# Kernel optimization log

Hardware: AMD Instinct MI355X
Metric: run time of the kernel (lower is better)

## Reference

```python
import jax, jax.numpy as jnp
import numpy as np

B, DIM, K, NH = 65536, 8, 64, 100
TOTAL = DIM * K


def setup_inputs() -> dict:
    key = jax.random.key(0)
    ks = jax.random.split(key, 14)
    e = jax.random.normal(ks[0], (B, DIM, K), dtype=jnp.float32)
    # strictly upper-triangular DAG adjacency: C[j, i] = 1 iff j < i (j is a parent of i)
    C = jnp.triu(jnp.ones((DIM, DIM), dtype=jnp.int32), k=1)
    sc = 0.05
    inp = {"e": e, "C": C}
    inp["sW1"] = jax.random.normal(ks[1], (TOTAL, NH), dtype=jnp.float32) * sc
    inp["sb1"] = jnp.zeros((NH,), dtype=jnp.float32)
    inp["sW2"] = jax.random.normal(ks[2], (NH, NH), dtype=jnp.float32) * sc
    inp["sb2"] = jnp.zeros((NH,), dtype=jnp.float32)
    inp["sW3"] = jax.random.normal(ks[3], (NH, K), dtype=jnp.float32) * sc
    inp["sb3"] = jnp.zeros((K,), dtype=jnp.float32)
    inp["tW1"] = jax.random.normal(ks[4], (TOTAL, NH), dtype=jnp.float32) * sc
    inp["tb1"] = jnp.zeros((NH,), dtype=jnp.float32)
    inp["tW2"] = jax.random.normal(ks[5], (NH, NH), dtype=jnp.float32) * sc
    inp["tb2"] = jnp.zeros((NH,), dtype=jnp.float32)
    inp["tW3"] = jax.random.normal(ks[6], (NH, K), dtype=jnp.float32) * sc
    inp["tb3"] = jnp.zeros((K,), dtype=jnp.float32)
    return inp


def _mlp(x, mask, W1, b1, W2, b2, W3, b3):
    # MLP.forward: net(x * mask); Linear->ReLU->Linear->ReLU->Linear->Sigmoid
    h = jax.nn.relu((x * mask) @ W1 + b1)
    h = jax.nn.relu(h @ W2 + b2)
    return jax.nn.sigmoid(h @ W3 + b3)


def reference(e, C, sW1, sb1, sW2, sb2, sW3, sb3, tW1, tb1, tW2, tb2, tW3, tb3):
    b, dim, k = e.shape
    total = dim * k
    # mask for step i: column C[:, i] with each entry repeated k times -> [total]
    # (if column i is all zeros, mask is zeros, matching the elif branch)
    masks = jnp.repeat(C.astype(e.dtype), k, axis=0).T  # [dim, total]
    e_steps = jnp.swapaxes(e, 0, 1)  # [dim, B, k]

    def step(z, xs):
        i, mask, e_i = xs
        zf = z.reshape(b, total)
        s = _mlp(zf, mask, sW1, sb1, sW2, sb2, sW3, sb3)  # [B, k]
        t = _mlp(zf, mask, tW1, tb1, tW2, tb2, tW3, tb3)  # [B, k]
        z = z.at[:, i, :].set(jnp.exp(s) * e_i + t)
        return z, jnp.sum(s, axis=1)

    z0 = jnp.zeros_like(e)
    z, ld_steps = jax.lax.scan(step, z0, (jnp.arange(dim), masks, e_steps))
    log_det = jnp.sum(ld_steps, axis=0)  # [B]
    return z, log_det
```

## Files before the change

### kernel.cpp

```cpp
#include <hip/hip_runtime.h>

#define B_SZ 65536
#define NH   100

typedef __bf16 bf16_t;
typedef __bf16 bf16x2 __attribute__((ext_vector_type(2)));
typedef __bf16 bf16x8 __attribute__((ext_vector_type(8)));
typedef float  f32x4  __attribute__((ext_vector_type(4)));

#define SZ_W2 14336
#define SZ_W3 8192
#define SZ_W1 7168
#define OFF_W3   28672
#define OFF_W1   45056
#define WS_TOTAL 145408

__global__ void prep_weights(const float* __restrict__ sW1, const float* __restrict__ sW2,
                             const float* __restrict__ sW3, const float* __restrict__ tW1,
                             const float* __restrict__ tW2, const float* __restrict__ tW3,
                             bf16_t* __restrict__ ws) {
  int idx = blockIdx.x * 256 + threadIdx.x;
  if (idx >= WS_TOTAL) return;
  float v = 0.f;
  if (idx < 2 * SZ_W2) {
    const float* W = (idx < SZ_W2) ? sW2 : tW2;
    int l = (idx < SZ_W2) ? idx : idx - SZ_W2;
    int j = l & 7, ln = (l >> 3) & 63, kc = (l >> 9) & 3, mt = l >> 11;
    int k = kc * 32 + (ln >> 4) * 8 + j;
    int m = mt * 16 + (ln & 15);
    v = (k < NH && m < NH) ? W[k * NH + m] : 0.f;
  } else if (idx < OFF_W1) {
    int l = idx - OFF_W3;
    const float* W = (l < SZ_W3) ? sW3 : tW3;
    l &= (SZ_W3 - 1);
    int j = l & 7, ln = (l >> 3) & 63, kc = (l >> 9) & 3, mt = l >> 11;
    int k = kc * 32 + (ln >> 4) * 8 + j;
    int m = mt * 16 + (ln & 15);
    v = (k < NH) ? W[k * 64 + m] : 0.f;
  } else {
    int l = idx - OFF_W1;
    int b = l / (2 * SZ_W1);
    int r2 = l - b * 2 * SZ_W1;
    const float* W = (r2 < SZ_W1) ? sW1 : tW1;
    int w = (r2 < SZ_W1) ? r2 : r2 - SZ_W1;
    int j = w & 7, ln = (w >> 3) & 63, kc = (w >> 9) & 1, mt = w >> 10;
    int k = kc * 32 + (ln >> 4) * 8 + j;
    int m = mt * 16 + (ln & 15);
    v = (m < NH) ? W[(b * 64 + k) * NH + m] : 0.f;
  }
  ws[idx] = (bf16_t)v;
}

__global__ void prep_bias(const float* __restrict__ sb1, const float* __restrict__ sb2,
                          const float* __restrict__ sb3, const float* __restrict__ tb1,
                          const float* __restrict__ tb2, const float* __restrict__ tb3,
                          float* __restrict__ fb) {
  int t = threadIdx.x;
  if (t < 112)       fb[t] = (t < NH) ? sb2[t] : 0.f;
  else if (t < 224)  fb[t] = (t - 112 < NH) ? tb2[t - 112] : 0.f;
  else if (t < 288)  fb[t] = sb3[t - 224];
  else if (t < 352)  fb[t] = tb3[t - 288];
  else if (t < 464)  fb[t] = (t - 352 < NH) ? sb1[t - 352] : 0.f;
  else if (t < 576)  fb[t] = (t - 464 < NH) ? tb1[t - 464] : 0.f;
}

__device__ __forceinline__ void gload_lds16(const void* gptr, void* lptr) {
  __builtin_amdgcn_global_load_lds(
      (const __attribute__((address_space(1))) unsigned int*)gptr,
      (__attribute__((address_space(3))) unsigned int*)lptr, 16, 0, 0);
}

__device__ __forceinline__ unsigned pk2(float a, float b) {
  bf16x2 t = {(bf16_t)a, (bf16_t)b};
  return __builtin_bit_cast(unsigned, t);
}

__device__ __forceinline__ void plswap(unsigned &x, unsigned &y) {
  asm("v_permlane32_swap_b32 %0, %1" : "+v"(x), "+v"(y));
  asm("v_permlane16_swap_b32 %0, %1" : "+v"(x), "+v"(y));
}

__device__ __forceinline__ bf16x8 build_bfrag(unsigned lo0, unsigned lo1,
                                              unsigned hi0, unsigned hi1) {
  plswap(lo0, hi0);
  plswap(lo1, hi1);
  union { unsigned u[4]; bf16x8 v; } r;
  r.u[0] = lo0; r.u[1] = lo1; r.u[2] = hi0; r.u[3] = hi1;
  return r.v;
}

struct __align__(16) SMem {
  bf16_t w2[2 * SZ_W2];
  bf16_t w3[2 * SZ_W3];
  float  bias[512];
};

__global__ __launch_bounds__(512, 2) void flow_kernel(
    const float* __restrict__ e,
    const bf16_t* __restrict__ wf,
    const float* __restrict__ fb,
    float* __restrict__ out) {
  __shared__ SMem sm;

  const int tid  = threadIdx.x;
  const int wave = tid >> 6;
  const int lane = tid & 63;
  const int c    = lane & 15;
  const int Q    = lane >> 4;
  const int rowBase = blockIdx.x * 256 + wave * 32;

  {
    const char* g = (const char*)wf;
    char* l = (char*)&sm;
    const char* gb = (const char*)fb;
    #pragma unroll
    for (int t = 0; t < 12; ++t) {
      const int ch = t * 8 + wave;
      if (ch < 88)      gload_lds16(g + ch * 1024 + lane * 16, l + ch * 1024);
      else if (ch < 90) gload_lds16(gb + (ch - 88) * 1024 + lane * 16,
                                    (char*)sm.bias + (ch - 88) * 1024);
    }
  }

  f32x4 acc1S[2][7], acc1T[2][7];
  #pragma unroll
  for (int th = 0; th < 7; ++th) {
    const f32x4 vs = *(const f32x4*)(fb + 352 + th * 16 + Q * 4);
    const f32x4 vt = *(const f32x4*)(fb + 464 + th * 16 + Q * 4);
    acc1S[0][th] = vs; acc1S[1][th] = vs;
    acc1T[0][th] = vt; acc1T[1][th] = vt;
  }
  float ldacc[2] = {0.f, 0.f};

  __syncthreads();

  const float* lb2S = sm.bias;
  const float* lb2T = sm.bias + 112;
  const float* lb3S = sm.bias + 224;
  const float* lb3T = sm.bias + 288;

  auto run_net = [&](const f32x4 (&acc1)[2][7], const bf16_t* __restrict__ w2f,
                     const bf16_t* __restrict__ w3f, const float* __restrict__ lb2,
                     const float* __restrict__ lb3, f32x4 (&acc3)[2][4]) {
    unsigned pk[2][7][2];
    #pragma unroll
    for (int mt = 0; mt < 2; ++mt)
      #pragma unroll
      for (int th = 0; th < 7; ++th) {
        pk[mt][th][0] = pk2(fmaxf(acc1[mt][th][0], 0.f), fmaxf(acc1[mt][th][1], 0.f));
        pk[mt][th][1] = pk2(fmaxf(acc1[mt][th][2], 0.f), fmaxf(acc1[mt][th][3], 0.f));
      }
    f32x4 acc2[2][7];
    #pragma unroll
    for (int th = 0; th < 7; ++th) {
      const f32x4 bv = *(const f32x4*)(lb2 + th * 16 + Q * 4);
      acc2[0][th] = bv; acc2[1][th] = bv;
    }
    #pragma unroll
    for (int kc = 0; kc < 4; ++kc) {
      const int tlo = kc * 2, thi = (kc * 2 + 1 > 6) ? 6 : kc * 2 + 1;
      const bf16x8 b0 = build_bfrag(pk[0][tlo][0], pk[0][tlo][1], pk[0][thi][0], pk[0][thi][1]);
      const bf16x8 b1 = build_bfrag(pk[1][tlo][0], pk[1][tlo][1], pk[1][thi][0], pk[1][thi][1]);
      #pragma unroll
      for (int th = 0; th < 7; ++th) {
        const bf16x8 A = *(const bf16x8*)(w2f + ((th * 4 + kc) * 64 + lane) * 8);
        acc2[0][th] = __builtin_amdgcn_mfma_f32_16x16x32_bf16(A, b0, acc2[0][th], 0, 0, 0);
        acc2[1][th] = __builtin_amdgcn_mfma_f32_16x16x32_bf16(A, b1, acc2[1][th], 0, 0, 0);
      }
    }
    #pragma unroll
    for (int mt = 0; mt < 2; ++mt)
      #pragma unroll
      for (int th = 0; th < 7; ++th) {
        pk[mt][th][0] = pk2(fmaxf(acc2[mt][th][0], 0.f), fmaxf(acc2[mt][th][1], 0.f));
        pk[mt][th][1] = pk2(fmaxf(acc2[mt][th][2], 0.f), fmaxf(acc2[mt][th][3], 0.f));
      }
    #pragma unroll
    for (int ot = 0; ot < 4; ++ot) {
      const f32x4 bv = *(const f32x4*)(lb3 + ot * 16 + Q * 4);
      acc3[0][ot] = bv; acc3[1][ot] = bv;
    }
    #pragma unroll
    for (int kc = 0; kc < 4; ++kc) {
      const int tlo = kc * 2, thi = (kc * 2 + 1 > 6) ? 6 : kc * 2 + 1;
      const bf16x8 b0 = build_bfrag(pk[0][tlo][0], pk[0][tlo][1], pk[0][thi][0], pk[0][thi][1]);
      const bf16x8 b1 = build_bfrag(pk[1][tlo][0], pk[1][tlo][1], pk[1][thi][0], pk[1][thi][1]);
      #pragma unroll
      for (int ot = 0; ot < 4; ++ot) {
        const bf16x8 A = *(const bf16x8*)(w3f + ((ot * 4 + kc) * 64 + lane) * 8);
        acc3[0][ot] = __builtin_amdgcn_mfma_f32_16x16x32_bf16(A, b0, acc3[0][ot], 0, 0, 0);
        acc3[1][ot] = __builtin_amdgcn_mfma_f32_16x16x32_bf16(A, b1, acc3[1][ot], 0, 0, 0);
      }
    }
  };

  for (int i = 0; i < 8; ++i) {
    f32x4 acc3S[2][4], acc3T[2][4];
    run_net(acc1S, sm.w2,         sm.w3,         lb2S, lb3S, acc3S);
    run_net(acc1T, sm.w2 + SZ_W2, sm.w3 + SZ_W3, lb2T, lb3T, acc3T);

    unsigned zpk[2][4][2];
    #pragma unroll
    for (int mt = 0; mt < 2; ++mt) {
      #pragma unroll
      for (int ot = 0; ot < 4; ++ot) {
        const int off = (rowBase + mt * 16 + c) * 512 + i * 64 + ot * 16 + Q * 4;
        const f32x4 ev = *(const f32x4*)(e + off);
        f32x4 zv;
        float ss = 0.f;
        #pragma unroll
        for (int r = 0; r < 4; ++r) {
          const float sv = __builtin_amdgcn_rcpf(1.f + __expf(-acc3S[mt][ot][r]));
          const float tv = __builtin_amdgcn_rcpf(1.f + __expf(-acc3T[mt][ot][r]));
          zv[r] = __expf(sv) * ev[r] + tv;
          ss += sv;
        }
        __builtin_nontemporal_store(zv, (f32x4*)(out + off));
        zpk[mt][ot][0] = pk2(zv[0], zv[1]);
        zpk[mt][ot][1] = pk2(zv[2], zv[3]);
        ldacc[mt] += ss;
      }
    }

    if (i < 7) {
      const bf16_t* __restrict__ w1g = wf + OFF_W1 + i * 2 * SZ_W1;
      #pragma unroll
      for (int kc = 0; kc < 2; ++kc) {
        const bf16x8 b0 = build_bfrag(zpk[0][kc * 2][0], zpk[0][kc * 2][1],
                                      zpk[0][kc * 2 + 1][0], zpk[0][kc * 2 + 1][1]);
        const bf16x8 b1 = build_bfrag(zpk[1][kc * 2][0], zpk[1][kc * 2][1],
                                      zpk[1][kc * 2 + 1][0], zpk[1][kc * 2 + 1][1]);
        #pragma unroll
        for (int th = 0; th < 7; ++th) {
          const bf16x8 AS = *(const bf16x8*)(w1g + ((th * 2 + kc) * 64 + lane) * 8);
          const bf16x8 AT = *(const bf16x8*)(w1g + SZ_W1 + ((th * 2 + kc) * 64 + lane) * 8);
          acc1S[0][th] = __builtin_amdgcn_mfma_f32_16x16x32_bf16(AS, b0, acc1S[0][th], 0, 0, 0);
          acc1S[1][th] = __builtin_amdgcn_mfma_f32_16x16x32_bf16(AS, b1, acc1S[1][th], 0, 0, 0);
          acc1T[0][th] = __builtin_amdgcn_mfma_f32_16x16x32_bf16(AT, b0, acc1T[0][th], 0, 0, 0);
          acc1T[1][th] = __builtin_amdgcn_mfma_f32_16x16x32_bf16(AT, b1, acc1T[1][th], 0, 0, 0);
        }
      }
    }
  }

  #pragma unroll
  for (int mt = 0; mt < 2; ++mt) {
    float v = ldacc[mt];
    v += __shfl_xor(v, 16);
    v += __shfl_xor(v, 32);
    if (Q == 0) out[B_SZ * 512 + rowBase + mt * 16 + c] = v;
  }
}

extern "C" void kernel_launch(void* const* d_in, const int* in_sizes, int n_in,
                              void* d_out, int out_size, void* d_ws, size_t ws_size,
                              hipStream_t stream) {
  (void)in_sizes; (void)n_in; (void)out_size; (void)ws_size;
  const float* e   = (const float*)d_in[0];
  const float* sW1 = (const float*)d_in[2];
  const float* sb1 = (const float*)d_in[3];
  const float* sW2 = (const float*)d_in[4];
  const float* sb2 = (const float*)d_in[5];
  const float* sW3 = (const float*)d_in[6];
  const float* sb3 = (const float*)d_in[7];
  const float* tW1 = (const float*)d_in[8];
  const float* tb1 = (const float*)d_in[9];
  const float* tW2 = (const float*)d_in[10];
  const float* tb2 = (const float*)d_in[11];
  const float* tW3 = (const float*)d_in[12];
  const float* tb3 = (const float*)d_in[13];
  bf16_t* ws = (bf16_t*)d_ws;
  float*  fb = (float*)(ws + WS_TOTAL);
  float* out = (float*)d_out;

  prep_weights<<<(WS_TOTAL + 255) / 256, 256, 0, stream>>>(sW1, sW2, sW3, tW1, tW2, tW3, ws);
  prep_bias<<<1, 576, 0, stream>>>(sb1, sb2, sb3, tb1, tb2, tb3, fb);
  flow_kernel<<<256, 512, 0, stream>>>(e, ws, fb, out);
}
```

Baseline: 393.2 us.

## Stage per-step W1 weights in double-buffered LDS with async prefetch

Per-step layer-1 weight tiles now go into two LDS buffers instead of being read straight from global memory. The next step's tile is prefetched with global_load_lds while the current step's MLPs run. A block-wide barrier is added before each W1 use, and LDS per block grows by about 56 KB. The permlane swaps switch to compiler builtins when available, and the layer-2/3 fragment-building index for the last chunk changes from 6 to 5, which alters which zero-padded data is used.

```diff
diff --git a/kernel.cpp b/kernel.cpp
--- a/kernel.cpp
+++ b/kernel.cpp
@@ -7,6 +7,7 @@
 typedef __bf16 bf16x2 __attribute__((ext_vector_type(2)));
 typedef __bf16 bf16x8 __attribute__((ext_vector_type(8)));
 typedef float  f32x4  __attribute__((ext_vector_type(4)));
+typedef unsigned u32x2 __attribute__((ext_vector_type(2)));
 
 #define SZ_W2 14336
 #define SZ_W3 8192
@@ -75,10 +76,25 @@
   return __builtin_bit_cast(unsigned, t);
 }
 
+#if __has_builtin(__builtin_amdgcn_permlane32_swap) && __has_builtin(__builtin_amdgcn_permlane16_swap)
 __device__ __forceinline__ void plswap(unsigned &x, unsigned &y) {
-  asm("v_permlane32_swap_b32 %0, %1" : "+v"(x), "+v"(y));
-  asm("v_permlane16_swap_b32 %0, %1" : "+v"(x), "+v"(y));
-}
+  u32x2 a = __builtin_amdgcn_permlane32_swap(x, y, false, false);
+  u32x2 b = __builtin_amdgcn_permlane16_swap(a[0], a[1], false, false);
+  x = b[0]; y = b[1];
+}
+#else
+__device__ __forceinline__ void plswap(unsigned &x, unsigned &y) {
+  unsigned xo, yo;
+  asm volatile("v_mov_b32 %0, %2\n\t"
+               "v_mov_b32 %1, %3\n\t"
+               "s_nop 1\n\t"
+               "v_permlane32_swap_b32 %0, %1\n\t"
+               "s_nop 1\n\t"
+               "v_permlane16_swap_b32 %0, %1"
+               : "=&v"(xo), "=&v"(yo) : "v"(x), "v"(y));
+  x = xo; y = yo;
+}
+#endif
 
 __device__ __forceinline__ bf16x8 build_bfrag(unsigned lo0, unsigned lo1,
                                               unsigned hi0, unsigned hi1) {
@@ -92,6 +108,7 @@
 struct __align__(16) SMem {
   bf16_t w2[2 * SZ_W2];
   bf16_t w3[2 * SZ_W3];
+  bf16_t w1[2][2 * SZ_W1];
   float  bias[512];
 };
 
@@ -114,11 +131,11 @@
     char* l = (char*)&sm;
     const char* gb = (const char*)fb;
     #pragma unroll
-    for (int t = 0; t < 12; ++t) {
+    for (int t = 0; t < 15; ++t) {
       const int ch = t * 8 + wave;
-      if (ch < 88)      gload_lds16(g + ch * 1024 + lane * 16, l + ch * 1024);
-      else if (ch < 90) gload_lds16(gb + (ch - 88) * 1024 + lane * 16,
-                                    (char*)sm.bias + (ch - 88) * 1024);
+      if (ch < 116)      gload_lds16(g + ch * 1024 + lane * 16, l + ch * 1024);
+      else if (ch < 118) gload_lds16(gb + (ch - 116) * 1024 + lane * 16,
+                                     (char*)sm.bias + (ch - 116) * 1024);
     }
   }
 
@@ -158,7 +175,7 @@
     }
     #pragma unroll
     for (int kc = 0; kc < 4; ++kc) {
-      const int tlo = kc * 2, thi = (kc * 2 + 1 > 6) ? 6 : kc * 2 + 1;
+      const int tlo = kc * 2, thi = (kc * 2 + 1 > 6) ? 5 : kc * 2 + 1;
       const bf16x8 b0 = build_bfrag(pk[0][tlo][0], pk[0][tlo][1], pk[0][thi][0], pk[0][thi][1]);
       const bf16x8 b1 = build_bfrag(pk[1][tlo][0], pk[1][tlo][1], pk[1][thi][0], pk[1][thi][1]);
       #pragma unroll
@@ -182,7 +199,7 @@
     }
     #pragma unroll
     for (int kc = 0; kc < 4; ++kc) {
-      const int tlo = kc * 2, thi = (kc * 2 + 1 > 6) ? 6 : kc * 2 + 1;
+      const int tlo = kc * 2, thi = (kc * 2 + 1 > 6) ? 5 : kc * 2 + 1;
       const bf16x8 b0 = build_bfrag(pk[0][tlo][0], pk[0][tlo][1], pk[0][thi][0], pk[0][thi][1]);
       const bf16x8 b1 = build_bfrag(pk[1][tlo][0], pk[1][tlo][1], pk[1][thi][0], pk[1][thi][1]);
       #pragma unroll
@@ -223,7 +240,8 @@
     }
 
     if (i < 7) {
-      const bf16_t* __restrict__ w1g = wf + OFF_W1 + i * 2 * SZ_W1;
+      __syncthreads();
+      const bf16_t* __restrict__ w1b = sm.w1[i & 1];
       #pragma unroll
       for (int kc = 0; kc < 2; ++kc) {
         const bf16x8 b0 = build_bfrag(zpk[0][kc * 2][0], zpk[0][kc * 2][1],
@@ -232,12 +250,21 @@
                                       zpk[1][kc * 2 + 1][0], zpk[1][kc * 2 + 1][1]);
         #pragma unroll
         for (int th = 0; th < 7; ++th) {
-          const bf16x8 AS = *(const bf16x8*)(w1g + ((th * 2 + kc) * 64 + lane) * 8);
-          const bf16x8 AT = *(const bf16x8*)(w1g + SZ_W1 + ((th * 2 + kc) * 64 + lane) * 8);
+          const bf16x8 AS = *(const bf16x8*)(w1b + ((th * 2 + kc) * 64 + lane) * 8);
+          const bf16x8 AT = *(const bf16x8*)(w1b + SZ_W1 + ((th * 2 + kc) * 64 + lane) * 8);
           acc1S[0][th] = __builtin_amdgcn_mfma_f32_16x16x32_bf16(AS, b0, acc1S[0][th], 0, 0, 0);
           acc1S[1][th] = __builtin_amdgcn_mfma_f32_16x16x32_bf16(AS, b1, acc1S[1][th], 0, 0, 0);
           acc1T[0][th] = __builtin_amdgcn_mfma_f32_16x16x32_bf16(AT, b0, acc1T[0][th], 0, 0, 0);
           acc1T[1][th] = __builtin_amdgcn_mfma_f32_16x16x32_bf16(AT, b1, acc1T[1][th], 0, 0, 0);
+        }
+      }
+      if (i < 6) {
+        const char* g = (const char*)wf + 90112 + (i + 1) * 28672;
+        char* l = (char*)sm.w1[(i + 1) & 1];
+        #pragma unroll
+        for (int t = 0; t < 4; ++t) {
+          const int ch = t * 8 + wave;
+          if (ch < 28) gload_lds16(g + ch * 1024 + lane * 16, l + ch * 1024);
         }
       }
     }
```

Measured after the change: 319.1 us. 1.23x faster.
